# Optimization experiments

Measured on AMD Instinct MI355X. Metric: run time of the kernel, lower is better.

Reference implementation:

```python
import jax, jax.numpy as jnp
import numpy as np

NUM_HEADS = 8


def _forward(x, Wq, bq, Wk, bk, Wv, bv, Wo, bo, w1, b1, w2, b2, tau):
    B, S, E = x.shape
    H = NUM_HEADS
    hd = E // H
    scale = hd ** -0.5

    def heads(t):
        return t.reshape(B, S, H, hd).transpose(0, 2, 1, 3)  # [B,H,S,hd]

    q = heads(x @ Wq + bq)
    k = heads(x @ Wk + bk)
    v = heads(x @ Wv + bv)
    s = jnp.einsum('bhqd,bhkd->bhqk', q, k) * scale  # [B,H,S,S]

    # ---- autopoietic transform (vectorized over batch, no mask) ----
    s = jnp.clip(jnp.nan_to_num(s, nan=0.0, posinf=10.0, neginf=-10.0), -15.0, 15.0)
    ma = s.mean(axis=1)  # mean over heads -> [B,S,S]
    eps_safe = 0.05  # clamp(eps=1e-6, 0.05, 0.8)
    sa = jnp.clip(jnp.clip(ma, -8.0, 8.0) * eps_safe, -10.0, 10.0)
    # 1x1 conv on [1,1,S,S] == per-channel scalar scale+bias -> [B,C,S,S]
    hid = jax.nn.relu(jnp.clip(sa[:, None] * w1[None, :, None, None]
                               + b1[None, :, None, None], -5.0, 5.0))
    ap = jnp.clip(jnp.einsum('bcij,c->bij', hid, w2) + b2, -5.0, 5.0)
    taylor = jnp.clip(1.0 + 0.05 * (ap * 50.0), 0.5, 1.5)
    sig = jax.nn.sigmoid(taylor)
    p = jax.nn.softmax(jnp.clip(ma, -10.0, 10.0), axis=-1)
    Hent = -p * jnp.log(p + 1e-6)
    Fm = jax.nn.softmax(3.0 * Hent, axis=-1)
    t = sig * Fm
    eo = jnp.sqrt((ma * ma).sum(axis=(1, 2), keepdims=True)) + 1e-4  # fro norm
    et = jnp.sqrt((t * t).sum(axis=(1, 2), keepdims=True)) + 1e-4
    t = jnp.clip(eo / et, 0.8, 1.2) * t
    tm = t.mean(axis=(1, 2), keepdims=True)
    om = ma.mean(axis=(1, 2), keepdims=True)
    tstd = jnp.sqrt(jnp.clip(((t - tm) ** 2).mean(axis=(1, 2), keepdims=True), 0.01, None))
    ostd = jnp.sqrt(jnp.clip(((ma - om) ** 2).mean(axis=(1, 2), keepdims=True), 0.01, None))
    gd = jnp.clip(ostd / tstd, 0.8, 1.2)
    ar = jnp.clip(jnp.abs(ma).max(axis=(1, 2), keepdims=True), 1.0, 10.0)
    sm = jnp.clip(0.3 / jnp.log1p(ar), 0.1, 0.5)
    st = tm + sm * gd * (t - tm)  # scaled_transform
    ent = Hent.mean(axis=(1, 2), keepdims=True)
    ne = ent / jnp.log(jnp.float32(S))  # normalized entropy (max_entropy = log S)
    rr = 0.4 * (1.0 - jnp.clip(ne, 0.0, 0.4))  # residual ratio (base 0.4, entropy-damped)
    # blend transform back into per-head scores (res_scale = 1.0)
    s = s + rr[:, None] * (st - ma)[:, None]

    attn = jax.nn.softmax(s / tau, axis=-1)
    out = jnp.einsum('bhqk,bhkd->bhqd', attn, v)
    out = out.transpose(0, 2, 1, 3).reshape(B, S, E)
    return out @ Wo + bo


def setup_inputs() -> dict:
    key = jax.random.key(0)
    ks = jax.random.split(key, 8)
    B, S, E, C = 4, 512, 512, 128
    w_scale = 0.02
    return {
        'x': jax.random.normal(ks[0], (B, S, E), dtype=jnp.float32),
        'Wq': jax.random.normal(ks[1], (E, E), dtype=jnp.float32) * w_scale,
        'bq': jnp.zeros((E,), jnp.float32),
        'Wk': jax.random.normal(ks[2], (E, E), dtype=jnp.float32) * w_scale,
        'bk': jnp.zeros((E,), jnp.float32),
        'Wv': jax.random.normal(ks[3], (E, E), dtype=jnp.float32) * w_scale,
        'bv': jnp.zeros((E,), jnp.float32),
        'Wo': jax.random.normal(ks[4], (E, E), dtype=jnp.float32) * w_scale,
        'bo': jnp.zeros((E,), jnp.float32),
        'w1': jax.random.normal(ks[5], (C,), dtype=jnp.float32) * 0.5,
        'b1': jnp.zeros((C,), jnp.float32),
        'w2': jax.random.normal(ks[6], (C,), dtype=jnp.float32) * 0.1,
        'b2': jnp.zeros((1,), jnp.float32),
        'tau': jnp.ones((1,), jnp.float32),
    }


def reference(x, Wq, bq, Wk, bk, Wv, bv, Wo, bo, w1, b1, w2, b2, tau):
    return _forward(x, Wq, bq, Wk, bk, Wv, bv, Wo, bo, w1, b1, w2, b2, tau)
```

## Files before the change

### kernel.cpp

```cpp
#include <hip/hip_runtime.h>
#include <math.h>

#define BB 4
#define SS 512
#define EE 512
#define NH 8
#define HD 64
#define NC 128
#define NTAB 4096

typedef _Float16 f16x8 __attribute__((ext_vector_type(8)));
typedef float f32x4 __attribute__((ext_vector_type(4)));

struct HL { _Float16 h, l; };

__device__ __forceinline__ float clampf(float v, float lo, float hi) {
  return fminf(fmaxf(v, lo), hi);
}
__device__ __forceinline__ HL split16(float x) {
  HL r;
  r.h = (_Float16)x;
  r.l = (_Float16)(x - (float)r.h);
  return r;
}

__device__ __forceinline__ float waveRedSum(float v) {
#pragma unroll
  for (int o = 32; o; o >>= 1) v += __shfl_xor(v, o);
  return v;
}
__device__ __forceinline__ float waveRedMax(float v) {
#pragma unroll
  for (int o = 32; o; o >>= 1) v = fmaxf(v, __shfl_xor(v, o));
  return v;
}
__device__ __forceinline__ float blockRedSum(float v, float* red) {
  int tid = threadIdx.x;
  v = waveRedSum(v);
  __syncthreads();
  if ((tid & 63) == 0) red[tid >> 6] = v;
  __syncthreads();
  return red[0] + red[1] + red[2] + red[3];
}
__device__ __forceinline__ float blockRedMax(float v, float* red) {
  int tid = threadIdx.x;
  v = waveRedMax(v);
  __syncthreads();
  if ((tid & 63) == 0) red[tid >> 6] = v;
  __syncthreads();
  return fmaxf(fmaxf(red[0], red[1]), fmaxf(red[2], red[3]));
}

__global__ __launch_bounds__(256) void k_prep(
    const float* __restrict__ Wq, const float* __restrict__ Wk,
    const float* __restrict__ Wv, const float* __restrict__ Wo,
    const float* __restrict__ x,
    _Float16* __restrict__ Wth, _Float16* __restrict__ Wtl,
    _Float16* __restrict__ xh) {
  const int j = blockIdx.x;
  const int tid = threadIdx.x;
  if (j >= 256) {
    const int rb = (j - 256) * 64;
    const int r = tid >> 2;
    const int c0 = (tid & 3) * 128;
    const float* src = x + (size_t)(rb + r) * EE + c0;
    _Float16* dst = xh + (size_t)(rb + r) * EE + c0;
#pragma unroll
    for (int c = 0; c < 128; c += 8) {
      float4 a = *(const float4*)(src + c);
      float4 b = *(const float4*)(src + c + 4);
      f16x8 h;
      h[0] = (_Float16)a.x; h[1] = (_Float16)a.y;
      h[2] = (_Float16)a.z; h[3] = (_Float16)a.w;
      h[4] = (_Float16)b.x; h[5] = (_Float16)b.y;
      h[6] = (_Float16)b.z; h[7] = (_Float16)b.w;
      *(f16x8*)(dst + c) = h;
    }
    return;
  }
  const int z = j >> 6;
  const int rem = j & 63;
  const int k0 = (rem & 7) * 64, n0 = (rem >> 3) * 64;
  const float* W = (z == 0) ? Wq : (z == 1) ? Wk : (z == 2) ? Wv : Wo;
  __shared__ float Tt[64][68];
  const int r = tid >> 2, c = (tid & 3) * 16;
#pragma unroll
  for (int jj = 0; jj < 16; jj += 4)
    *(float4*)&Tt[r][c + jj] =
        *(const float4*)(W + (size_t)(k0 + r) * EE + n0 + c + jj);
  __syncthreads();
  f16x8 h0, l0, h1, l1;
#pragma unroll
  for (int jj = 0; jj < 8; ++jj) {
    HL r0 = split16(Tt[c + jj][r]);
    HL r1 = split16(Tt[c + 8 + jj][r]);
    h0[jj] = r0.h; l0[jj] = r0.l;
    h1[jj] = r1.h; l1[jj] = r1.l;
  }
  _Float16* dh = Wth + ((size_t)z * EE + n0 + r) * EE + k0 + c;
  _Float16* dl = Wtl + ((size_t)z * EE + n0 + r) * EE + k0 + c;
  *(f16x8*)dh = h0;
  *(f16x8*)(dh + 8) = h1;
  *(f16x8*)dl = l0;
  *(f16x8*)(dl + 8) = l1;
}

__global__ __launch_bounds__(256) void k_qkv_mfma(
    const _Float16* __restrict__ xh,
    const _Float16* __restrict__ Wth, const _Float16* __restrict__ Wtl,
    const float* __restrict__ bq, const float* __restrict__ bk,
    const float* __restrict__ bv, const float* __restrict__ w1,
    const float* __restrict__ b1, const float* __restrict__ w2,
    const float* __restrict__ b2, float* __restrict__ T,
    _Float16* __restrict__ qh,
    _Float16* __restrict__ kh, _Float16* __restrict__ kl,
    _Float16* __restrict__ vth, _Float16* __restrict__ vtl) {
  const int which = blockIdx.z;
  const int tid = threadIdx.x;
  const int wave = tid >> 6, lane = tid & 63;
  const int quad = lane >> 4, l16 = lane & 15;
  const int m0 = blockIdx.y * 64;
  const int n0 = blockIdx.x * 64;
  const _Float16* Bh = Wth + (size_t)which * EE * EE;
  const _Float16* Bl = Wtl + (size_t)which * EE * EE;

  __shared__ __align__(16) char smpool[27648];
  _Float16(*LAh)[72] = (_Float16(*)[72])(smpool);
  _Float16(*LBh)[72] = (_Float16(*)[72])(smpool + 9216);
  _Float16(*LBl)[72] = (_Float16(*)[72])(smpool + 18432);
  float(*TR)[68] = (float(*)[68])(smpool);

  const int sr0 = tid >> 3, sc0 = (tid & 7) * 8;
  const int sr1 = sr0 + 32;

  f16x8 rA0h = *(const f16x8*)(xh + (size_t)(m0 + sr0) * EE + sc0);
  f16x8 rA1h = *(const f16x8*)(xh + (size_t)(m0 + sr1) * EE + sc0);
  f16x8 rB0h = *(const f16x8*)(Bh + (size_t)(n0 + sr0) * EE + sc0);
  f16x8 rB0l = *(const f16x8*)(Bl + (size_t)(n0 + sr0) * EE + sc0);
  f16x8 rB1h = *(const f16x8*)(Bh + (size_t)(n0 + sr1) * EE + sc0);
  f16x8 rB1l = *(const f16x8*)(Bl + (size_t)(n0 + sr1) * EE + sc0);

  f32x4 acc[4] = {};
  for (int k0 = 0; k0 < EE; k0 += 64) {
    if (k0) __syncthreads();
    *(f16x8*)&LAh[sr0][sc0] = rA0h;
    *(f16x8*)&LAh[sr1][sc0] = rA1h;
    *(f16x8*)&LBh[sr0][sc0] = rB0h;
    *(f16x8*)&LBl[sr0][sc0] = rB0l;
    *(f16x8*)&LBh[sr1][sc0] = rB1h;
    *(f16x8*)&LBl[sr1][sc0] = rB1l;
    __syncthreads();
    if (k0 + 64 < EE) {
      const int kn = k0 + 64;
      rA0h = *(const f16x8*)(xh + (size_t)(m0 + sr0) * EE + kn + sc0);
      rA1h = *(const f16x8*)(xh + (size_t)(m0 + sr1) * EE + kn + sc0);
      rB0h = *(const f16x8*)(Bh + (size_t)(n0 + sr0) * EE + kn + sc0);
      rB0l = *(const f16x8*)(Bl + (size_t)(n0 + sr0) * EE + kn + sc0);
      rB1h = *(const f16x8*)(Bh + (size_t)(n0 + sr1) * EE + kn + sc0);
      rB1l = *(const f16x8*)(Bl + (size_t)(n0 + sr1) * EE + kn + sc0);
    }
#pragma unroll
    for (int kk = 0; kk < 64; kk += 32) {
      f16x8 ah = *(const f16x8*)&LAh[wave * 16 + l16][kk + quad * 8];
#pragma unroll
      for (int nt = 0; nt < 4; ++nt) {
        f16x8 bhf = *(const f16x8*)&LBh[nt * 16 + l16][kk + quad * 8];
        f16x8 blf = *(const f16x8*)&LBl[nt * 16 + l16][kk + quad * 8];
        acc[nt] = __builtin_amdgcn_mfma_f32_16x16x32_f16(ah, bhf, acc[nt], 0, 0, 0);
        acc[nt] = __builtin_amdgcn_mfma_f32_16x16x32_f16(ah, blf, acc[nt], 0, 0, 0);
      }
    }
  }
  const float* bias = (which == 0) ? bq : (which == 1) ? bk : bv;
  if (which == 2) {
    __syncthreads();
#pragma unroll
    for (int nt = 0; nt < 4; ++nt) {
      const int dcol = nt * 16 + l16;
      const float bb = bias[n0 + nt * 16 + l16];
#pragma unroll
      for (int r = 0; r < 4; ++r)
        TR[dcol][wave * 16 + quad * 4 + r] = acc[nt][r] + bb;
    }
    __syncthreads();
    const int d = tid >> 2, cc = (tid & 3) * 16;
    const int bh = (m0 >> 9) * NH + (n0 >> 6);
    const int si0 = m0 & 511;
    f16x8 h0, l0, h1, l1;
#pragma unroll
    for (int jj = 0; jj < 8; ++jj) {
      HL r0 = split16(TR[d][cc + jj]);
      HL r1 = split16(TR[d][cc + 8 + jj]);
      h0[jj] = r0.h; l0[jj] = r0.l;
      h1[jj] = r1.h; l1[jj] = r1.l;
    }
    _Float16* dh = vth + ((size_t)bh * HD + d) * SS + si0 + cc;
    _Float16* dl = vtl + ((size_t)bh * HD + d) * SS + si0 + cc;
    *(f16x8*)dh = h0;
    *(f16x8*)(dh + 8) = h1;
    *(f16x8*)dl = l0;
    *(f16x8*)(dl + 8) = l1;
  } else {
    const float postscale = (which == 0) ? 0.125f : 1.0f;
    const int mbase = m0 + wave * 16 + quad * 4;
#pragma unroll
    for (int nt = 0; nt < 4; ++nt) {
      const int col = n0 + nt * 16 + l16;
      const float bb = bias[col];
#pragma unroll
      for (int r = 0; r < 4; ++r) {
        const size_t idx = (size_t)(mbase + r) * EE + col;
        const float val = (acc[nt][r] + bb) * postscale;
        if (which == 0) {
          qh[idx] = (_Float16)val;
        } else {
          HL sp = split16(val);
          kh[idx] = sp.h;
          kl[idx] = sp.l;
        }
      }
    }
    if (which == 0 && blockIdx.x == 0 && blockIdx.y < 17) {
      int idx = blockIdx.y * 256 + tid;
      if (idx <= NTAB) {
        float sa = -0.4f + (float)idx * (0.8f / (float)NTAB);
        float ap = 0.f;
#pragma unroll 4
        for (int c = 0; c < NC; ++c) {
          float h = fminf(fmaxf(sa * w1[c] + b1[c], 0.f), 5.f);
          ap += h * w2[c];
        }
        ap = clampf(ap + b2[0], -5.f, 5.f);
        float tay = clampf(1.0f + 0.05f * (ap * 50.0f), 0.5f, 1.5f);
        T[idx] = 1.0f / (1.0f + expf(-tay));
      }
    }
  }
}

__global__ __launch_bounds__(256) void k_ma_mfma(
    const _Float16* __restrict__ qh,
    const _Float16* __restrict__ kh, const _Float16* __restrict__ kl,
    _Float16* __restrict__ ma) {
  const int tid = threadIdx.x;
  const int wave = tid >> 6, lane = tid & 63;
  const int quad = lane >> 4, l16 = lane & 15;
  const int m0 = blockIdx.y * 64;
  const int n0 = blockIdx.x * 64;
  const _Float16* Bh = kh + (size_t)(m0 >> 9) * SS * EE;
  const _Float16* Bl = kl + (size_t)(m0 >> 9) * SS * EE;

  __shared__ _Float16 LAh[64][72], LBh[64][72], LBl[64][72];

  const int sr0 = tid >> 3, sc0 = (tid & 7) * 8;
  const int sr1 = sr0 + 32;

  f16x8 rA0h = *(const f16x8*)(qh + (size_t)(m0 + sr0) * EE + sc0);
  f16x8 rB0h = *(const f16x8*)(Bh + (size_t)(n0 + sr0) * EE + sc0);
  f16x8 rB0l = *(const f16x8*)(Bl + (size_t)(n0 + sr0) * EE + sc0);
  f16x8 rA1h = *(const f16x8*)(qh + (size_t)(m0 + sr1) * EE + sc0);
  f16x8 rB1h = *(const f16x8*)(Bh + (size_t)(n0 + sr1) * EE + sc0);
  f16x8 rB1l = *(const f16x8*)(Bl + (size_t)(n0 + sr1) * EE + sc0);

  f32x4 acc[4] = {};
  for (int k0 = 0; k0 < EE; k0 += 64) {
    if (k0) __syncthreads();
    *(f16x8*)&LAh[sr0][sc0] = rA0h;
    *(f16x8*)&LBh[sr0][sc0] = rB0h;
    *(f16x8*)&LBl[sr0][sc0] = rB0l;
    *(f16x8*)&LAh[sr1][sc0] = rA1h;
    *(f16x8*)&LBh[sr1][sc0] = rB1h;
    *(f16x8*)&LBl[sr1][sc0] = rB1l;
    __syncthreads();
    if (k0 + 64 < EE) {
      const int kn = k0 + 64;
      rA0h = *(const f16x8*)(qh + (size_t)(m0 + sr0) * EE + kn + sc0);
      rB0h = *(const f16x8*)(Bh + (size_t)(n0 + sr0) * EE + kn + sc0);
      rB0l = *(const f16x8*)(Bl + (size_t)(n0 + sr0) * EE + kn + sc0);
      rA1h = *(const f16x8*)(qh + (size_t)(m0 + sr1) * EE + kn + sc0);
      rB1h = *(const f16x8*)(Bh + (size_t)(n0 + sr1) * EE + kn + sc0);
      rB1l = *(const f16x8*)(Bl + (size_t)(n0 + sr1) * EE + kn + sc0);
    }
#pragma unroll
    for (int kk = 0; kk < 64; kk += 32) {
      f16x8 ah = *(const f16x8*)&LAh[wave * 16 + l16][kk + quad * 8];
#pragma unroll
      for (int nt = 0; nt < 4; ++nt) {
        f16x8 bhf = *(const f16x8*)&LBh[nt * 16 + l16][kk + quad * 8];
        f16x8 blf = *(const f16x8*)&LBl[nt * 16 + l16][kk + quad * 8];
        acc[nt] = __builtin_amdgcn_mfma_f32_16x16x32_f16(ah, bhf, acc[nt], 0, 0, 0);
        acc[nt] = __builtin_amdgcn_mfma_f32_16x16x32_f16(ah, blf, acc[nt], 0, 0, 0);
      }
    }
  }
  const int mbase = m0 + wave * 16 + quad * 4;
#pragma unroll
  for (int nt = 0; nt < 4; ++nt) {
    const int col = n0 + nt * 16 + l16;
#pragma unroll
    for (int r = 0; r < 4; ++r) {
      ma[(size_t)(mbase + r) * SS + col] = (_Float16)(acc[nt][r] * 0.125f);
    }
  }
}

__global__ __launch_bounds__(256) void k_rowstat(
    const _Float16* __restrict__ ma, const float* __restrict__ T,
    _Float16* __restrict__ t_un, float* __restrict__ rowred) {
  const int row = blockIdx.x * 4 + (threadIdx.x >> 6);
  const int lane = threadIdx.x & 63;

  f16x8 mv8 = *(const f16x8*)(ma + (size_t)row * SS + lane * 8);
  float m[8];
#pragma unroll
  for (int e = 0; e < 8; ++e) m[e] = (float)mv8[e];

  float sma = 0.f, sma2 = 0.f, mabs = 0.f;
#pragma unroll
  for (int e = 0; e < 8; ++e) {
    sma += m[e];
    sma2 += m[e] * m[e];
    mabs = fmaxf(mabs, fabsf(m[e]));
  }
  sma = waveRedSum(sma);
  sma2 = waveRedSum(sma2);
  mabs = waveRedMax(mabs);

  float ex[8], esum = 0.f;
#pragma unroll
  for (int e = 0; e < 8; ++e) {
    ex[e] = __expf(clampf(m[e], -10.f, 10.f));
    esum += ex[e];
  }
  esum = waveRedSum(esum);
  float inv = 1.0f / esum;
  float Hv[8], sH = 0.f;
#pragma unroll
  for (int e = 0; e < 8; ++e) {
    float pp = ex[e] * inv;
    Hv[e] = -pp * __logf(pp + 1e-6f);
    sH += Hv[e];
  }
  sH = waveRedSum(sH);

  float fx[8], fsum = 0.f;
#pragma unroll
  for (int e = 0; e < 8; ++e) {
    fx[e] = __expf(3.0f * Hv[e]);
    fsum += fx[e];
  }
  fsum = waveRedSum(fsum);
  float finv = 1.0f / fsum;

  float t[8], st = 0.f, st2 = 0.f;
#pragma unroll
  for (int e = 0; e < 8; ++e) {
    float sa = clampf(m[e], -8.f, 8.f) * 0.05f;
    float pos = (sa + 0.4f) * ((float)NTAB / 0.8f);
    int idx = (int)pos;
    idx = idx < 0 ? 0 : (idx > NTAB - 1 ? NTAB - 1 : idx);
    float frac = pos - (float)idx;
    float g0 = T[idx], g1 = T[idx + 1];
    float sig = g0 + (g1 - g0) * frac;
    t[e] = sig * fx[e] * finv;
    st += t[e];
    st2 += t[e] * t[e];
  }
  st = waveRedSum(st);
  st2 = waveRedSum(st2);
  {
    f16x8 tw;
#pragma unroll
    for (int e = 0; e < 8; ++e) tw[e] = (_Float16)t[e];
    *(f16x8*)(t_un + (size_t)row * SS + lane * 8) = tw;
  }
  if (lane == 0) {
    float* rp = rowred + (size_t)row * 8;
    rp[0] = sma; rp[1] = sma2; rp[2] = mabs;
    rp[3] = st;  rp[4] = st2;  rp[5] = sH;
  }
}

__global__ __launch_bounds__(256) void k_consts(
    const float* __restrict__ rowred, float* __restrict__ cvec) {
  const int b_ = blockIdx.x;
  const int tid = threadIdx.x;
  __shared__ float red[4];
  const float* r0 = rowred + ((size_t)b_ * SS + tid * 2) * 8;
  const float* r1 = r0 + 8;
  float sma = blockRedSum(r0[0] + r1[0], red);
  float sma2 = blockRedSum(r0[1] + r1[1], red);
  float mabs = blockRedMax(fmaxf(r0[2], r1[2]), red);
  float st = blockRedSum(r0[3] + r1[3], red);
  float st2 = blockRedSum(r0[4] + r1[4], red);
  float sH = blockRedSum(r0[5] + r1[5], red);
  if (tid == 0) {
    const float N = (float)(SS * SS);
    float eo = sqrtf(sma2) + 1e-4f;
    float et = sqrtf(st2) + 1e-4f;
    float r = clampf(eo / et, 0.8f, 1.2f);
    float tmean = r * st / N;
    float om = sma / N;
    float vart = r * r * fmaxf(st2 / N - (st / N) * (st / N), 0.f);
    float tstd = sqrtf(fmaxf(vart, 0.01f));
    float varo = fmaxf(sma2 / N - om * om, 0.f);
    float ostd = sqrtf(fmaxf(varo, 0.01f));
    float gd = clampf(ostd / tstd, 0.8f, 1.2f);
    float ar = clampf(mabs, 1.f, 10.f);
    float sm = clampf(0.3f / log1pf(ar), 0.1f, 0.5f);
    float ent = sH / N;
    float ne = ent / logf((float)SS);
    float rr = 0.4f * (1.f - clampf(ne, 0.f, 0.4f));
    float G = sm * gd;
    cvec[b_ * 4 + 0] = rr * (1.f - G) * tmean;
    cvec[b_ * 4 + 1] = rr * G * r;
    cvec[b_ * 4 + 2] = rr;
  }
}

__global__ __launch_bounds__(256) void k_av_fused(
    const _Float16* __restrict__ qh,
    const _Float16* __restrict__ kh, const _Float16* __restrict__ kl,
    const _Float16* __restrict__ ma, const _Float16* __restrict__ t_un,
    const float* __restrict__ cvec, const float* __restrict__ tau,
    const _Float16* __restrict__ vth, const _Float16* __restrict__ vtl,
    _Float16* __restrict__ oh) {
  const int bh = blockIdx.y;
  const int b_ = bh >> 3, hh = bh & 7;
  const int m0 = blockIdx.x * 16;
  const int tid = threadIdx.x;
  const int wave = tid >> 6, lane = tid & 63;
  const int quad = lane >> 4, l16 = lane & 15;

  const float c0 = cvec[b_ * 4 + 0];
  const float c1 = cvec[b_ * 4 + 1];
  const float c2 = cvec[b_ * 4 + 2];
  const float itau = 1.0f / tau[0];

  __shared__ _Float16 Ph[16][72];
  __shared__ float Zp[16][4];

  const size_t qbase = (size_t)(b_ * SS + m0 + l16) * EE + hh * HD;
  f16x8 a_hi[2];
#pragma unroll
  for (int s2 = 0; s2 < 2; ++s2)
    a_hi[s2] = *(const f16x8*)(qh + qbase + s2 * 32 + quad * 8);

  const size_t kbase = (size_t)b_ * SS * EE + hh * HD;
  const size_t vbase = ((size_t)bh * HD + wave * 16 + l16) * SS;
  const size_t mb0 =
      (size_t)(b_ * SS + m0 + quad * 4) * SS + wave * 16 + l16;

  f16x8 kb_h[2], kb_l[2], vb_h[2], vb_l[2];
  _Float16 mv[4], tv[4];
  {
    const size_t kr = kbase + (size_t)(wave * 16 + l16) * EE;
#pragma unroll
    for (int s2 = 0; s2 < 2; ++s2) {
      kb_h[s2] = *(const f16x8*)(kh + kr + s2 * 32 + quad * 8);
      kb_l[s2] = *(const f16x8*)(kl + kr + s2 * 32 + quad * 8);
    }
#pragma unroll
    for (int vs = 0; vs < 2; ++vs) {
      vb_h[vs] = *(const f16x8*)(vth + vbase + vs * 32 + quad * 8);
      vb_l[vs] = *(const f16x8*)(vtl + vbase + vs * 32 + quad * 8);
    }
#pragma unroll
    for (int r = 0; r < 4; ++r) {
      mv[r] = ma[mb0 + (size_t)r * SS];
      tv[r] = t_un[mb0 + (size_t)r * SS];
    }
  }

  float z[4] = {0.f, 0.f, 0.f, 0.f};
  f32x4 oacc = {};
  for (int k0 = 0; k0 < SS; k0 += 64) {
    f32x4 qacc = {};
#pragma unroll
    for (int s2 = 0; s2 < 2; ++s2) {
      qacc = __builtin_amdgcn_mfma_f32_16x16x32_f16(a_hi[s2], kb_h[s2], qacc, 0, 0, 0);
      qacc = __builtin_amdgcn_mfma_f32_16x16x32_f16(a_hi[s2], kb_l[s2], qacc, 0, 0, 0);
    }
    const f16x8 vh_c0 = vb_h[0], vh_c1 = vb_h[1];
    const f16x8 vl_c0 = vb_l[0], vl_c1 = vb_l[1];
    __syncthreads();
#pragma unroll
    for (int r = 0; r < 4; ++r) {
      float sc = clampf(qacc[r], -15.f, 15.f);
      float v = (sc + c0 + c1 * (float)tv[r] - c2 * (float)mv[r]) * itau;
      float e = __expf(v) * 1.52587890625e-05f;
      z[r] += e;
      Ph[quad * 4 + r][wave * 16 + l16] = (_Float16)e;
    }
    if (k0 + 64 < SS) {
      const int kn = k0 + 64;
      const size_t kr = kbase + (size_t)(kn + wave * 16 + l16) * EE;
#pragma unroll
      for (int s2 = 0; s2 < 2; ++s2) {
        kb_h[s2] = *(const f16x8*)(kh + kr + s2 * 32 + quad * 8);
        kb_l[s2] = *(const f16x8*)(kl + kr + s2 * 32 + quad * 8);
      }
#pragma unroll
      for (int vs = 0; vs < 2; ++vs) {
        vb_h[vs] = *(const f16x8*)(vth + vbase + kn + vs * 32 + quad * 8);
        vb_l[vs] = *(const f16x8*)(vtl + vbase + kn + vs * 32 + quad * 8);
      }
#pragma unroll
      for (int r = 0; r < 4; ++r) {
        mv[r] = ma[mb0 + (size_t)r * SS + kn];
        tv[r] = t_un[mb0 + (size_t)r * SS + kn];
      }
    }
    __syncthreads();
    {
      f16x8 ah0 = *(const f16x8*)&Ph[l16][quad * 8];
      f16x8 ah1 = *(const f16x8*)&Ph[l16][32 + quad * 8];
      oacc = __builtin_amdgcn_mfma_f32_16x16x32_f16(ah0, vh_c0, oacc, 0, 0, 0);
      oacc = __builtin_amdgcn_mfma_f32_16x16x32_f16(ah0, vl_c0, oacc, 0, 0, 0);
      oacc = __builtin_amdgcn_mfma_f32_16x16x32_f16(ah1, vh_c1, oacc, 0, 0, 0);
      oacc = __builtin_amdgcn_mfma_f32_16x16x32_f16(ah1, vl_c1, oacc, 0, 0, 0);
    }
  }
#pragma unroll
  for (int off = 1; off < 16; off <<= 1) {
#pragma unroll
    for (int r = 0; r < 4; ++r) z[r] += __shfl_xor(z[r], off);
  }
  if (l16 == 0) {
#pragma unroll
    for (int r = 0; r < 4; ++r) Zp[quad * 4 + r][wave] = z[r];
  }
  __syncthreads();
#pragma unroll
  for (int r = 0; r < 4; ++r) {
    const int lr = quad * 4 + r;
    const float Z = Zp[lr][0] + Zp[lr][1] + Zp[lr][2] + Zp[lr][3];
    const float oV = oacc[r] / Z;
    const size_t idx =
        ((size_t)(b_ * SS + m0 + lr)) * EE + hh * HD + wave * 16 + l16;
    oh[idx] = (_Float16)oV;
  }
}

__global__ __launch_bounds__(256) void k_out_mfma(
    const _Float16* __restrict__ oh,
    const _Float16* __restrict__ Wth, const _Float16* __restrict__ Wtl,
    const float* __restrict__ bo, float* __restrict__ out) {
  const int tid = threadIdx.x;
  const int wave = tid >> 6, lane = tid & 63;
  const int quad = lane >> 4, l16 = lane & 15;
  const int m0 = blockIdx.y * 64;
  const int n0 = blockIdx.x * 64;
  const _Float16* Bh = Wth + (size_t)3 * EE * EE;
  const _Float16* Bl = Wtl + (size_t)3 * EE * EE;

  __shared__ _Float16 LAh[64][72], LBh[64][72], LBl[64][72];

  const int sr0 = tid >> 3, sc0 = (tid & 7) * 8;
  const int sr1 = sr0 + 32;

  f16x8 rA0h = *(const f16x8*)(oh + (size_t)(m0 + sr0) * EE + sc0);
  f16x8 rB0h = *(const f16x8*)(Bh + (size_t)(n0 + sr0) * EE + sc0);
  f16x8 rB0l = *(const f16x8*)(Bl + (size_t)(n0 + sr0) * EE + sc0);
  f16x8 rA1h = *(const f16x8*)(oh + (size_t)(m0 + sr1) * EE + sc0);
  f16x8 rB1h = *(const f16x8*)(Bh + (size_t)(n0 + sr1) * EE + sc0);
  f16x8 rB1l = *(const f16x8*)(Bl + (size_t)(n0 + sr1) * EE + sc0);

  f32x4 acc[4] = {};
  for (int k0 = 0; k0 < EE; k0 += 64) {
    if (k0) __syncthreads();
    *(f16x8*)&LAh[sr0][sc0] = rA0h;
    *(f16x8*)&LBh[sr0][sc0] = rB0h;
    *(f16x8*)&LBl[sr0][sc0] = rB0l;
    *(f16x8*)&LAh[sr1][sc0] = rA1h;
    *(f16x8*)&LBh[sr1][sc0] = rB1h;
    *(f16x8*)&LBl[sr1][sc0] = rB1l;
    __syncthreads();
    if (k0 + 64 < EE) {
      const int kn = k0 + 64;
      rA0h = *(const f16x8*)(oh + (size_t)(m0 + sr0) * EE + kn + sc0);
      rB0h = *(const f16x8*)(Bh + (size_t)(n0 + sr0) * EE + kn + sc0);
      rB0l = *(const f16x8*)(Bl + (size_t)(n0 + sr0) * EE + kn + sc0);
      rA1h = *(const f16x8*)(oh + (size_t)(m0 + sr1) * EE + kn + sc0);
      rB1h = *(const f16x8*)(Bh + (size_t)(n0 + sr1) * EE + kn + sc0);
      rB1l = *(const f16x8*)(Bl + (size_t)(n0 + sr1) * EE + kn + sc0);
    }
#pragma unroll
    for (int kk = 0; kk < 64; kk += 32) {
      f16x8 ah = *(const f16x8*)&LAh[wave * 16 + l16][kk + quad * 8];
#pragma unroll
      for (int nt = 0; nt < 4; ++nt) {
        f16x8 bhf = *(const f16x8*)&LBh[nt * 16 + l16][kk + quad * 8];
        f16x8 blf = *(const f16x8*)&LBl[nt * 16 + l16][kk + quad * 8];
        acc[nt] = __builtin_amdgcn_mfma_f32_16x16x32_f16(ah, bhf, acc[nt], 0, 0, 0);
        acc[nt] = __builtin_amdgcn_mfma_f32_16x16x32_f16(ah, blf, acc[nt], 0, 0, 0);
      }
    }
  }
  const int mbase = m0 + wave * 16 + quad * 4;
#pragma unroll
  for (int nt = 0; nt < 4; ++nt) {
    const int col = n0 + nt * 16 + l16;
    const float bb = bo[col];
#pragma unroll
    for (int r = 0; r < 4; ++r) {
      const int m = mbase + r;
      out[(size_t)m * EE + col] = acc[nt][r] + bb;
    }
  }
}

extern "C" void kernel_launch(void* const* d_in, const int* in_sizes, int n_in,
                              void* d_out, int out_size, void* d_ws,
                              size_t ws_size, hipStream_t stream) {
  const float* x = (const float*)d_in[0];
  const float* Wq = (const float*)d_in[1];
  const float* bq = (const float*)d_in[2];
  const float* Wk = (const float*)d_in[3];
  const float* bk = (const float*)d_in[4];
  const float* Wv = (const float*)d_in[5];
  const float* bv = (const float*)d_in[6];
  const float* Wo = (const float*)d_in[7];
  const float* bo = (const float*)d_in[8];
  const float* w1 = (const float*)d_in[9];
  const float* b1 = (const float*)d_in[10];
  const float* w2 = (const float*)d_in[11];
  const float* b2 = (const float*)d_in[12];
  const float* tau = (const float*)d_in[13];
  float* out = (float*)d_out;

  const size_t NX = (size_t)2048 * EE;
  const size_t NW = (size_t)4 * EE * EE;
  const size_t NQK = (size_t)BB * SS * EE;
  const size_t NSS = (size_t)BB * SS * SS;

  _Float16* Wth = (_Float16*)d_ws;
  _Float16* Wtl = Wth + NW;
  _Float16* xh = Wtl + NW;
  _Float16* qh = xh + NX;
  _Float16* kh = qh + NQK;
  _Float16* kl = kh + NQK;
  _Float16* vth = kl + NQK;
  _Float16* vtl = vth + NQK;
  _Float16* oh = vtl + NQK;
  _Float16* ma = oh + NX;
  _Float16* t_un = ma + NSS;
  float* T = (float*)(t_un + NSS);
  float* rowred = T + 8192;
  float* cvec = rowred + 2048 * 8;

  k_prep<<<288, 256, 0, stream>>>(Wq, Wk, Wv, Wo, x, Wth, Wtl, xh);
  k_qkv_mfma<<<dim3(8, 32, 3), 256, 0, stream>>>(xh, Wth, Wtl, bq, bk, bv, w1,
                                                 b1, w2, b2, T, qh, kh, kl,
                                                 vth, vtl);
  k_ma_mfma<<<dim3(8, 32), 256, 0, stream>>>(qh, kh, kl, ma);
  k_rowstat<<<512, 256, 0, stream>>>(ma, T, t_un, rowred);
  k_consts<<<4, 256, 0, stream>>>(rowred, cvec);
  k_av_fused<<<dim3(32, 32), 256, 0, stream>>>(qh, kh, kl, ma, t_un, cvec,
                                               tau, vth, vtl, oh);
  k_out_mfma<<<dim3(8, 32), 256, 0, stream>>>(oh, Wth, Wtl, bo, out);
}
```

Before: 167.7 us.

## Split key range across waves in fused attention-AV kernel to remove per-step barriers

Each wave now handles its own 128-key slice for all 64 head dims, with private LDS staging for P, instead of all waves sharing a 64-key step and synchronizing twice per step. Partial outputs and normalizers are reduced across waves through LDS once at the end. This removes the per-iteration __syncthreads and the cross-wave dependency. In exchange it adds more registers for four accumulators, drops the software prefetch of the next tile, and adds a final LDS reduction.

Result: no change. 168.0 us (+0.2%).

```diff
diff --git a/kernel.cpp b/kernel.cpp
--- a/kernel.cpp
+++ b/kernel.cpp
@@ -431,114 +431,109 @@
   const int tid = threadIdx.x;
   const int wave = tid >> 6, lane = tid & 63;
   const int quad = lane >> 4, l16 = lane & 15;
+  const int cbeg = wave * 128;
 
   const float c0 = cvec[b_ * 4 + 0];
   const float c1 = cvec[b_ * 4 + 1];
   const float c2 = cvec[b_ * 4 + 2];
   const float itau = 1.0f / tau[0];
 
-  __shared__ _Float16 Ph[16][72];
-  __shared__ float Zp[16][4];
+  __shared__ __align__(16) _Float16 Ph[4][16][40];
+  __shared__ __align__(16) float Olds[4][16][68];
+  __shared__ float Zlds[4][16];
 
   const size_t qbase = (size_t)(b_ * SS + m0 + l16) * EE + hh * HD;
   f16x8 a_hi[2];
 #pragma unroll
-  for (int s2 = 0; s2 < 2; ++s2)
-    a_hi[s2] = *(const f16x8*)(qh + qbase + s2 * 32 + quad * 8);
+  for (int ks = 0; ks < 2; ++ks)
+    a_hi[ks] = *(const f16x8*)(qh + qbase + ks * 32 + quad * 8);
 
   const size_t kbase = (size_t)b_ * SS * EE + hh * HD;
-  const size_t vbase = ((size_t)bh * HD + wave * 16 + l16) * SS;
-  const size_t mb0 =
-      (size_t)(b_ * SS + m0 + quad * 4) * SS + wave * 16 + l16;
-
-  f16x8 kb_h[2], kb_l[2], vb_h[2], vb_l[2];
-  _Float16 mv[4], tv[4];
+  const size_t vbase = ((size_t)bh * HD + l16) * SS;
+  const size_t mrow = (size_t)(b_ * SS + m0 + quad * 4) * SS;
+
+  float z[4] = {0.f, 0.f, 0.f, 0.f};
+  f32x4 oacc[4] = {};
+  for (int c0i = cbeg; c0i < cbeg + 128; c0i += 32) {
+    f16x8 kbh[2][2], kbl[2][2];
+#pragma unroll
+    for (int ct = 0; ct < 2; ++ct) {
+      const size_t kr = kbase + (size_t)(c0i + ct * 16 + l16) * EE;
+#pragma unroll
+      for (int ks = 0; ks < 2; ++ks) {
+        kbh[ct][ks] = *(const f16x8*)(kh + kr + ks * 32 + quad * 8);
+        kbl[ct][ks] = *(const f16x8*)(kl + kr + ks * 32 + quad * 8);
+      }
+    }
+    f16x8 vbh[4], vbl[4];
+#pragma unroll
+    for (int dt = 0; dt < 4; ++dt) {
+      const size_t vr = vbase + (size_t)(dt * 16) * SS + c0i + quad * 8;
+      vbh[dt] = *(const f16x8*)(vth + vr);
+      vbl[dt] = *(const f16x8*)(vtl + vr);
+    }
+    _Float16 mv[2][4], tv[2][4];
+#pragma unroll
+    for (int ct = 0; ct < 2; ++ct)
+#pragma unroll
+      for (int r = 0; r < 4; ++r) {
+        const size_t off = mrow + (size_t)r * SS + c0i + ct * 16 + l16;
+        mv[ct][r] = ma[off];
+        tv[ct][r] = t_un[off];
+      }
+#pragma unroll
+    for (int ct = 0; ct < 2; ++ct) {
+      f32x4 qacc = {};
+#pragma unroll
+      for (int ks = 0; ks < 2; ++ks) {
+        qacc = __builtin_amdgcn_mfma_f32_16x16x32_f16(a_hi[ks], kbh[ct][ks], qacc, 0, 0, 0);
+        qacc = __builtin_amdgcn_mfma_f32_16x16x32_f16(a_hi[ks], kbl[ct][ks], qacc, 0, 0, 0);
+      }
+#pragma unroll
+      for (int r = 0; r < 4; ++r) {
+        float sc = clampf(qacc[r], -15.f, 15.f);
+        float v = (sc + c0 + c1 * (float)tv[ct][r] - c2 * (float)mv[ct][r]) * itau;
+        float e = __expf(v) * 1.52587890625e-05f;
+        z[r] += e;
+        Ph[wave][quad * 4 + r][ct * 16 + l16] = (_Float16)e;
+      }
+    }
+    f16x8 pa = *(const f16x8*)&Ph[wave][l16][quad * 8];
+#pragma unroll
+    for (int dt = 0; dt < 4; ++dt) {
+      oacc[dt] = __builtin_amdgcn_mfma_f32_16x16x32_f16(pa, vbh[dt], oacc[dt], 0, 0, 0);
+      oacc[dt] = __builtin_amdgcn_mfma_f32_16x16x32_f16(pa, vbl[dt], oacc[dt], 0, 0, 0);
+    }
+  }
+#pragma unroll
+  for (int off = 1; off < 16; off <<= 1) {
+#pragma unroll
+    for (int r = 0; r < 4; ++r) z[r] += __shfl_xor(z[r], off);
+  }
+  if (l16 == 0) {
+#pragma unroll
+    for (int r = 0; r < 4; ++r) Zlds[wave][quad * 4 + r] = z[r];
+  }
+#pragma unroll
+  for (int dt = 0; dt < 4; ++dt)
+#pragma unroll
+    for (int r = 0; r < 4; ++r)
+      Olds[wave][quad * 4 + r][dt * 16 + l16] = oacc[dt][r];
+  __syncthreads();
   {
-    const size_t kr = kbase + (size_t)(wave * 16 + l16) * EE;
-#pragma unroll
-    for (int s2 = 0; s2 < 2; ++s2) {
-      kb_h[s2] = *(const f16x8*)(kh + kr + s2 * 32 + quad * 8);
-      kb_l[s2] = *(const f16x8*)(kl + kr + s2 * 32 + quad * 8);
-    }
-#pragma unroll
-    for (int vs = 0; vs < 2; ++vs) {
-      vb_h[vs] = *(const f16x8*)(vth + vbase + vs * 32 + quad * 8);
-      vb_l[vs] = *(const f16x8*)(vtl + vbase + vs * 32 + quad * 8);
-    }
-#pragma unroll
-    for (int r = 0; r < 4; ++r) {
-      mv[r] = ma[mb0 + (size_t)r * SS];
-      tv[r] = t_un[mb0 + (size_t)r * SS];
-    }
-  }
-
-  float z[4] = {0.f, 0.f, 0.f, 0.f};
-  f32x4 oacc = {};
-  for (int k0 = 0; k0 < SS; k0 += 64) {
-    f32x4 qacc = {};
-#pragma unroll
-    for (int s2 = 0; s2 < 2; ++s2) {
-      qacc = __builtin_amdgcn_mfma_f32_16x16x32_f16(a_hi[s2], kb_h[s2], qacc, 0, 0, 0);
-      qacc = __builtin_amdgcn_mfma_f32_16x16x32_f16(a_hi[s2], kb_l[s2], qacc, 0, 0, 0);
-    }
-    const f16x8 vh_c0 = vb_h[0], vh_c1 = vb_h[1];
-    const f16x8 vl_c0 = vb_l[0], vl_c1 = vb_l[1];
-    __syncthreads();
-#pragma unroll
-    for (int r = 0; r < 4; ++r) {
-      float sc = clampf(qacc[r], -15.f, 15.f);
-      float v = (sc + c0 + c1 * (float)tv[r] - c2 * (float)mv[r]) * itau;
-      float e = __expf(v) * 1.52587890625e-05f;
-      z[r] += e;
-      Ph[quad * 4 + r][wave * 16 + l16] = (_Float16)e;
-    }
-    if (k0 + 64 < SS) {
-      const int kn = k0 + 64;
-      const size_t kr = kbase + (size_t)(kn + wave * 16 + l16) * EE;
-#pragma unroll
-      for (int s2 = 0; s2 < 2; ++s2) {
-        kb_h[s2] = *(const f16x8*)(kh + kr + s2 * 32 + quad * 8);
-        kb_l[s2] = *(const f16x8*)(kl + kr + s2 * 32 + quad * 8);
-      }
-#pragma unroll
-      for (int vs = 0; vs < 2; ++vs) {
-        vb_h[vs] = *(const f16x8*)(vth + vbase + kn + vs * 32 + quad * 8);
-        vb_l[vs] = *(const f16x8*)(vtl + vbase + kn + vs * 32 + quad * 8);
-      }
-#pragma unroll
-      for (int r = 0; r < 4; ++r) {
-        mv[r] = ma[mb0 + (size_t)r * SS + kn];
-        tv[r] = t_un[mb0 + (size_t)r * SS + kn];
-      }
-    }
-    __syncthreads();
-    {
-      f16x8 ah0 = *(const f16x8*)&Ph[l16][quad * 8];
-      f16x8 ah1 = *(const f16x8*)&Ph[l16][32 + quad * 8];
-      oacc = __builtin_amdgcn_mfma_f32_16x16x32_f16(ah0, vh_c0, oacc, 0, 0, 0);
-      oacc = __builtin_amdgcn_mfma_f32_16x16x32_f16(ah0, vl_c0, oacc, 0, 0, 0);
-      oacc = __builtin_amdgcn_mfma_f32_16x16x32_f16(ah1, vh_c1, oacc, 0, 0, 0);
-      oacc = __builtin_amdgcn_mfma_f32_16x16x32_f16(ah1, vl_c1, oacc, 0, 0, 0);
-    }
-  }
-#pragma unroll
-  for (int off = 1; off < 16; off <<= 1) {
-#pragma unroll
-    for (int r = 0; r < 4; ++r) z[r] += __shfl_xor(z[r], off);
-  }
-  if (l16 == 0) {
-#pragma unroll
-    for (int r = 0; r < 4; ++r) Zp[quad * 4 + r][wave] = z[r];
-  }
-  __syncthreads();
-#pragma unroll
-  for (int r = 0; r < 4; ++r) {
-    const int lr = quad * 4 + r;
-    const float Z = Zp[lr][0] + Zp[lr][1] + Zp[lr][2] + Zp[lr][3];
-    const float oV = oacc[r] / Z;
-    const size_t idx =
-        ((size_t)(b_ * SS + m0 + lr)) * EE + hh * HD + wave * 16 + l16;
-    oh[idx] = (_Float16)oV;
+    const int row = tid >> 4;
+    const int d0 = (tid & 15) * 4;
+    float4 s0 = *(const float4*)&Olds[0][row][d0];
+    float4 s1 = *(const float4*)&Olds[1][row][d0];
+    float4 s2 = *(const float4*)&Olds[2][row][d0];
+    float4 s3 = *(const float4*)&Olds[3][row][d0];
+    float Z = Zlds[0][row] + Zlds[1][row] + Zlds[2][row] + Zlds[3][row];
+    float rz = 1.0f / Z;
+    _Float16* dst = oh + ((size_t)(b_ * SS + m0 + row)) * EE + hh * HD + d0;
+    dst[0] = (_Float16)((s0.x + s1.x + s2.x + s3.x) * rz);
+    dst[1] = (_Float16)((s0.y + s1.y + s2.y + s3.y) * rz);
+    dst[2] = (_Float16)((s0.z + s1.z + s2.z + s3.z) * rz);
+    dst[3] = (_Float16)((s0.w + s1.w + s2.w + s3.w) * rz);
   }
 }
 
```
